# Kernel tuning notes

Measured on AMD Instinct MI355X. Metric: run time of the kernel, lower is better.

The kernel has to match this reference:

```python
import jax, jax.numpy as jnp
import numpy as np

DIM = 768
HEADS = 12
HEAD_DIM = DIM // HEADS
SCALE = HEAD_DIM ** (-0.5)
BATCH = 1
SEQ = 4096


def setup_inputs() -> dict:
    key = jax.random.key(0)
    ks = jax.random.split(key, 5)
    x = jax.random.normal(ks[0], (BATCH, SEQ, DIM), dtype=jnp.float32)
    # Linear params stored (in, out) for y = x @ W + b
    w_qkv = jax.random.normal(ks[1], (DIM, 3 * DIM), dtype=jnp.float32) * (DIM ** -0.5)
    b_qkv = jnp.zeros((3 * DIM,), dtype=jnp.float32)
    w_proj = jax.random.normal(ks[2], (DIM, DIM), dtype=jnp.float32) * (DIM ** -0.5)
    b_proj = jnp.zeros((DIM,), dtype=jnp.float32)
    return {"x": x, "w_qkv": w_qkv, "b_qkv": b_qkv, "w_proj": w_proj, "b_proj": b_proj}


def reference(x, w_qkv, b_qkv, w_proj, b_proj):
    B, S, _ = x.shape
    qkv = x @ w_qkv + b_qkv                              # [B,S,3*DIM]
    qkv = qkv.reshape(B, S, 3, HEADS, HEAD_DIM)
    q, k, v = qkv[:, :, 0], qkv[:, :, 1], qkv[:, :, 2]   # [B,S,H,D]
    # scaled dot-product attention, full score matrix as in the original
    attn = jnp.einsum("bqhd,bkhd->bhqk", q * SCALE, k)   # [B,H,S,S]
    attn = jax.nn.softmax(attn, axis=-1)
    out = jnp.einsum("bhqk,bkhd->bqhd", attn, v)         # [B,S,H,D]
    out = out.reshape(B, S, DIM)
    return out @ w_proj + b_proj
```

## Files before the change

kernel.cpp:

```cpp
#include <hip/hip_runtime.h>
#include <hip/hip_bf16.h>

#define SEQ   4096
#define DIM   768
#define HEADS 12
#define NQKV  2304
#define QSCALE 0.18033688011f

#if __has_builtin(__builtin_amdgcn_exp2f)
#define EXP2(x) __builtin_amdgcn_exp2f(x)
#else
#define EXP2(x) __expf((x) * 0.69314718056f)
#endif

typedef __bf16 bf16_t;
typedef bf16_t bf16x8 __attribute__((ext_vector_type(8)));
typedef float  f32x4  __attribute__((ext_vector_type(4)));
typedef float  f32x16 __attribute__((ext_vector_type(16)));
typedef unsigned short u16;
typedef unsigned int   u32;

static __device__ __forceinline__ float bf2f(u16 v) {
    union { float f; unsigned u; } x; x.u = ((unsigned)v) << 16; return x.f;
}
static __device__ __forceinline__ u16 f2bf(float f) {
    union { float f; unsigned u; } x; x.f = f;
    unsigned r = x.u + 0x7fff + ((x.u >> 16) & 1);
    return (u16)(r >> 16);
}
static __device__ __forceinline__ u32 fbits(float f) {
    union { float f; unsigned u; } x; x.f = f; return x.u;
}
static __device__ __forceinline__ void gload_lds16(const u16* g, u16* l) {
    __builtin_amdgcn_global_load_lds(
        (const __attribute__((address_space(1))) unsigned int*)g,
        (__attribute__((address_space(3))) unsigned int*)l, 16, 0, 0);
}

static __device__ __forceinline__ int detect_f32(const u32* __restrict__ x) {
    int lane = threadIdx.x & 63;
    int cnt = 0;
#pragma unroll
    for (int i = 0; i < 8; ++i) {
        u32 w = x[lane * 8 + i];
        cnt += (((w >> 7) & 0xFF) >= 0x8F) ? 1 : 0;
    }
#pragma unroll
    for (int m = 1; m < 64; m <<= 1) cnt += __shfl_xor(cnt, m);
    return cnt >= 64;
}

__global__ __launch_bounds__(256) void prep(
    const void* __restrict__ x, const void* __restrict__ wqkv,
    const void* __restrict__ bqkv, const void* __restrict__ wproj,
    const void* __restrict__ bproj,
    u16* __restrict__ cvt, u16* __restrict__ wqkvT, u16* __restrict__ wprojT)
{
    __shared__ u16 tile[64][65];
    const bool f32 = detect_f32((const u32*)x) != 0;
    const int b = blockIdx.x;
    const int t = threadIdx.x;

    if (b < 576) {
        const void* src; u16* dst; int K, N, tx, ty;
        if (b < 432) { src = wqkv; dst = wqkvT; K = DIM; N = NQKV; tx = b % 36; ty = b / 36; }
        else { int bb = b - 432; src = wproj; dst = wprojT; K = DIM; N = DIM; tx = bb % 12; ty = bb / 12; }
        const int k0 = ty * 64, n0 = tx * 64;
#pragma unroll
        for (int i = 0; i < 4; ++i) {
            int idx = i * 256 + t;
            int r = idx >> 4, c4 = (idx & 15) * 4;
            size_t si = (size_t)(k0 + r) * N + n0 + c4;
            if (f32) {
                float4 v = *(const float4*)((const float*)src + si);
                tile[r][c4 + 0] = f2bf(v.x); tile[r][c4 + 1] = f2bf(v.y);
                tile[r][c4 + 2] = f2bf(v.z); tile[r][c4 + 3] = f2bf(v.w);
            } else {
                ushort4 v = *(const ushort4*)((const u16*)src + si);
                tile[r][c4 + 0] = v.x; tile[r][c4 + 1] = v.y;
                tile[r][c4 + 2] = v.z; tile[r][c4 + 3] = v.w;
            }
        }
        __syncthreads();
#pragma unroll
        for (int i = 0; i < 2; ++i) {
            int idx = i * 256 + t;
            int r = idx >> 3, c0 = (idx & 7) * 8;
            union { u16 u[8]; bf16x8 v; } pk;
#pragma unroll
            for (int j = 0; j < 8; ++j) pk.u[j] = tile[c0 + j][r];
            *(bf16x8*)(dst + (size_t)(n0 + r) * K + k0 + c0) = pk.v;
        }
    } else {
        const int SX = SEQ * DIM;
        const int gid = (b - 576) * 256 + t;
        for (int i = gid; i < SX / 8; i += 200 * 256) {
            if (f32) {
                float4 v0 = *((const float4*)x + (size_t)i * 2);
                float4 v1 = *((const float4*)x + (size_t)i * 2 + 1);
                union { u16 u[8]; bf16x8 v; } pk;
                pk.u[0] = f2bf(v0.x); pk.u[1] = f2bf(v0.y);
                pk.u[2] = f2bf(v0.z); pk.u[3] = f2bf(v0.w);
                pk.u[4] = f2bf(v1.x); pk.u[5] = f2bf(v1.y);
                pk.u[6] = f2bf(v1.z); pk.u[7] = f2bf(v1.w);
                *((bf16x8*)cvt + i) = pk.v;
            } else {
                *((bf16x8*)cvt + i) = *((const bf16x8*)x + i);
            }
        }
        if (gid < NQKV + DIM) {
            const void* s; int off;
            if (gid < NQKV) { s = bqkv;  off = gid; }
            else            { s = bproj; off = gid - NQKV; }
            cvt[SX + gid] = f32 ? f2bf(((const float*)s)[off]) : ((const u16*)s)[off];
        }
    }
}

template<int MODE, int BM, int BN>
__global__ __launch_bounds__(256) void gemm128(
    const u16* __restrict__ A, const u16* __restrict__ BT, const u16* __restrict__ bias,
    u16* __restrict__ C0, float* __restrict__ Cf, u16* __restrict__ VT,
    const u32* __restrict__ xdet, int M, int N, int K)
{
    constexpr int WM  = BM / 2;
    constexpr int WN  = BN / 2;
    constexpr int NI  = WM / 16;
    constexpr int NJ  = WN / 16;
    constexpr int ARW = BM / 4;
    constexpr int BRW = BN / 4;
    constexpr int LPS = (BM + BN) / 64;
    constexpr int TSTR = BM + 8;

    __shared__ union SharedLds {
        struct { u16 a[3][BM * 32]; u16 b[3][BN * 32]; } s;
        u16 t[(MODE == 1) ? 128 * TSTR : 1];
    } lds;

    const int t    = threadIdx.x;
    const int w    = t >> 6;
    const int lane = t & 63;
    const int l15  = lane & 15;
    const int quad = lane >> 4;
    const int wm   = w >> 1, wn = w & 1;

    const int lin     = blockIdx.y * gridDim.x + blockIdx.x;
    const int cpx     = (gridDim.x * gridDim.y) >> 3;
    const int logical = (lin & 7) * cpx + (lin >> 3);
    const int m0 = (logical / gridDim.x) * BM;
    const int n0 = (logical % gridDim.x) * BN;

    const int kch = (lane & 3) * 8;
    const u16* asrc = A  + (size_t)(m0 + w * ARW + (lane >> 2)) * K + kch;
    const u16* bsrc = BT + (size_t)(n0 + w * BRW + (lane >> 2)) * K + kch;
    const int woffA = w * ARW * 32;
    const int woffB = w * BRW * 32;

    f32x4 acc[NI][NJ] = {};

    u16 *aA = lds.s.a[0], *aB = lds.s.a[1], *aC = lds.s.a[2];
    u16 *bA = lds.s.b[0], *bB = lds.s.b[1], *bC = lds.s.b[2];

    auto STAGE = [&](u16* ad, u16* bd) {
#pragma unroll
        for (int s = 0; s < BM / 64; ++s)
            gload_lds16(asrc + s * 16 * K, ad + woffA + s * 16 * 32);
#pragma unroll
        for (int s = 0; s < BN / 64; ++s)
            gload_lds16(bsrc + s * 16 * K, bd + woffB + s * 16 * 32);
        asrc += 32; bsrc += 32;
    };
    auto COMPUTE = [&](const u16* ab_, const u16* bb_) {
        const u16* ab = ab_ + (wm * WM + l15) * 32 + quad * 8;
        const u16* bb = bb_ + (wn * WN + l15) * 32 + quad * 8;
        bf16x8 af[NI], bfr[NJ];
#pragma unroll
        for (int i = 0; i < NI; ++i) af[i]  = *(const bf16x8*)(ab + i * 16 * 32);
#pragma unroll
        for (int j = 0; j < NJ; ++j) bfr[j] = *(const bf16x8*)(bb + j * 16 * 32);
#pragma unroll
        for (int i = 0; i < NI; ++i)
#pragma unroll
            for (int j = 0; j < NJ; ++j)
                acc[i][j] = __builtin_amdgcn_mfma_f32_16x16x32_bf16(af[i], bfr[j], acc[i][j], 0, 0, 0);
    };
    auto WAIT_LPS = [&]() {
        if constexpr (LPS == 4)      asm volatile("s_waitcnt vmcnt(4)" ::: "memory");
        else if constexpr (LPS == 3) asm volatile("s_waitcnt vmcnt(3)" ::: "memory");
        else                         asm volatile("s_waitcnt vmcnt(2)" ::: "memory");
    };

    const int NK = K >> 5;
    STAGE(aA, bA);
    STAGE(aB, bB);
    for (int kt = 0; kt < NK - 2; ++kt) {
        WAIT_LPS();
        __builtin_amdgcn_s_barrier();
        STAGE(aC, bC);
        COMPUTE(aA, bA);
        { u16* tt = aA; aA = aB; aB = aC; aC = tt; }
        { u16* tt = bA; bA = bB; bB = bC; bC = tt; }
    }
    WAIT_LPS();
    __builtin_amdgcn_s_barrier();
    COMPUTE(aA, bA);
    { u16* tt = aA; aA = aB; aB = aC; aC = tt; }
    { u16* tt = bA; bA = bB; bB = bC; bC = tt; }
    asm volatile("s_waitcnt vmcnt(0)" ::: "memory");
    __builtin_amdgcn_s_barrier();
    COMPUTE(aA, bA);

    if constexpr (MODE == 1) {
        if (n0 >= 1536) {
            __syncthreads();
#pragma unroll
            for (int i = 0; i < NI; ++i)
#pragma unroll
                for (int j = 0; j < NJ; ++j)
#pragma unroll
                    for (int r = 0; r < 4; ++r) {
                        int ml = wm * WM + i * 16 + quad * 4 + r;
                        int nl = wn * WN + j * 16 + l15;
                        int mpl = (ml & ~15) | (ml & 3) |
                                  (((ml >> 2) & 1) << 3) | (((ml >> 3) & 1) << 2);
                        float v = acc[i][j][r] + bf2f(bias[n0 + nl]);
                        lds.t[nl * TSTR + mpl] = f2bf(v);
                    }
            __syncthreads();
            constexpr int LPR = BM / 8;
            constexpr int RPP = 256 / LPR;
            const int rr = t / LPR;
            const int mo = (t % LPR) * 8;
#pragma unroll
            for (int it = 0; it < 128 / RPP; ++it) {
                int nl = rr + it * RPP;
                *(bf16x8*)(VT + (size_t)(n0 - 1536 + nl) * SEQ + m0 + mo) =
                    *(const bf16x8*)(lds.t + nl * TSTR + mo);
            }
            return;
        }
    }

    bool outf32 = false;
    if (MODE == 0) outf32 = detect_f32(xdet) != 0;
#pragma unroll
    for (int i = 0; i < NI; ++i)
#pragma unroll
        for (int j = 0; j < NJ; ++j)
#pragma unroll
            for (int r = 0; r < 4; ++r) {
                int m = m0 + wm * WM + i * 16 + quad * 4 + r;
                int n = n0 + wn * WN + j * 16 + l15;
                float v = acc[i][j][r] + bf2f(bias[n]);
                if (MODE == 0) {
                    if (outf32) Cf[(size_t)m * N + n] = v;
                    else        C0[(size_t)m * N + n] = f2bf(v);
                } else {
                    float s = (n < 768) ? v * QSCALE : v;
                    C0[(size_t)m * 1536 + n] = f2bf(s);
                }
            }
}

__global__ __launch_bounds__(256, 3) void attn_kernel(
    const u16* __restrict__ qk, const u16* __restrict__ vt, u16* __restrict__ out)
{
    __shared__ u16 k_lds[3][64 * 64];
    __shared__ u16 v_lds[3][64 * 64];
    __shared__ float l_red[2][2][32];

    const int t    = threadIdx.x;
    const int w    = t >> 6;
    const int lane = t & 63;
    const int l31  = lane & 31;
    const int h    = lane >> 5;
    const int wq   = w & 1;
    const int wk   = w >> 1;

    const int lin     = blockIdx.x + (blockIdx.y << 6);
    const int logical = (lin & 7) * 96 + (lin >> 3);
    const int head    = logical >> 6;
    const int q0      = (logical & 63) * 64 + wq * 32;

    const u16* qrow = qk + (size_t)(q0 + l31) * 1536 + head * 64 + h * 8;
    bf16x8 qb[4];
#pragma unroll
    for (int s = 0; s < 4; ++s) qb[s] = *(const bf16x8*)(qrow + 16 * s);

    bf16x8 ones;
#pragma unroll
    for (int j = 0; j < 8; ++j) ones[j] = (bf16_t)1.0f;

    const f32x16 fz = {};

    const int srow = 8 * w + (lane >> 3);
    const int cs   = ((lane & 7) - srow) & 7;
    const u16* kst0 = qk + 768 + head * 64 + (size_t)srow * 1536 + cs * 8;
    const u16* kst1 = kst0 + (size_t)32 * 1536;
    const u16* vst0 = vt + (size_t)head * 64 * SEQ + (size_t)srow * SEQ + cs * 8;
    const u16* vst1 = vst0 + (size_t)32 * SEQ;
    const int woff = 8 * w * 64;

    const int krow = 32 * wk + l31;

    f32x16 o0 = {}, o1 = {}, lac = {};

    auto SK = [&](u16* kd) {
        gload_lds16(kst0, kd + woff);
        gload_lds16(kst1, kd + woff + 32 * 64);
        kst0 += (size_t)64 * 1536;
        kst1 += (size_t)64 * 1536;
    };
    auto SV = [&](u16* vd) {
        gload_lds16(vst0, vd + woff);
        gload_lds16(vst1, vd + woff + 32 * 64);
        vst0 += 64;
        vst1 += 64;
    };

    auto QK = [&](const u16* kb) -> f32x16 {
        const u16* kbase = kb + krow * 64;
        bf16x8 ka0 = *(const bf16x8*)(kbase + (((0 + h + krow) & 7) * 8));
        bf16x8 ka1 = *(const bf16x8*)(kbase + (((2 + h + krow) & 7) * 8));
        bf16x8 ka2 = *(const bf16x8*)(kbase + (((4 + h + krow) & 7) * 8));
        bf16x8 ka3 = *(const bf16x8*)(kbase + (((6 + h + krow) & 7) * 8));
        __builtin_amdgcn_s_setprio(1);
        f32x16 st = __builtin_amdgcn_mfma_f32_32x32x16_bf16(ka0, qb[0], fz, 0, 0, 0);
        st = __builtin_amdgcn_mfma_f32_32x32x16_bf16(ka1, qb[1], st, 0, 0, 0);
        st = __builtin_amdgcn_mfma_f32_32x32x16_bf16(ka2, qb[2], st, 0, 0, 0);
        st = __builtin_amdgcn_mfma_f32_32x32x16_bf16(ka3, qb[3], st, 0, 0, 0);
        __builtin_amdgcn_s_setprio(0);
        return st;
    };

    auto SMPV = [&](const f32x16& st, const u16* vb) {
        u32 q32[8];
#pragma unroll
        for (int i = 0; i < 8; ++i) {
            float pe = EXP2(st[2 * i]);
            float po = EXP2(st[2 * i + 1]);
            q32[i] = __builtin_amdgcn_perm(fbits(po), fbits(pe), 0x07060302u);
        }
        union { u32 u[4]; bf16x8 v; } pf0, pf1;
#pragma unroll
        for (int i = 0; i < 4; ++i) { pf0.u[i] = q32[i]; pf1.u[i] = q32[4 + i]; }
        __builtin_amdgcn_s_setprio(1);
#pragma unroll
        for (int s2 = 0; s2 < 2; ++s2) {
            const int c = 4 * wk + 2 * s2 + h;
            bf16x8 vb0 = *(const bf16x8*)(vb + l31 * 64 + (((c + l31) & 7) * 8));
            bf16x8 vb1 = *(const bf16x8*)(vb + (32 + l31) * 64 + (((c + 32 + l31) & 7) * 8));
            const bf16x8 pv = s2 ? pf1.v : pf0.v;
            o0  = __builtin_amdgcn_mfma_f32_32x32x16_bf16(pv, vb0, o0, 0, 0, 0);
            o1  = __builtin_amdgcn_mfma_f32_32x32x16_bf16(pv, vb1, o1, 0, 0, 0);
            lac = __builtin_amdgcn_mfma_f32_32x32x16_bf16(pv, ones, lac, 0, 0, 0);
        }
        __builtin_amdgcn_s_setprio(0);
    };

    u16 *kA = &k_lds[0][0], *kB = &k_lds[1][0], *kC = &k_lds[2][0];
    u16 *vA = &v_lds[0][0], *vB = &v_lds[1][0], *vC = &v_lds[2][0];

    SK(kA);
    SV(vA);
    SK(kB);
    asm volatile("s_waitcnt vmcnt(4)" ::: "memory");
    __builtin_amdgcn_s_barrier();
    f32x16 stA = QK(kA);
    SV(vB);
    f32x16 stB;

    for (int i = 0; i < 31; ++i) {
        SK(kC);
        asm volatile("s_waitcnt vmcnt(4)" ::: "memory");
        __builtin_amdgcn_s_barrier();
        stB = QK(kB);
        SMPV(stA, vA);
        SV(vC);
        { u16* tt = kA; kA = kB; kB = kC; kC = tt; }
        { u16* tt = vA; vA = vB; vB = vC; vC = tt; }
        SK(kC);
        asm volatile("s_waitcnt vmcnt(4)" ::: "memory");
        __builtin_amdgcn_s_barrier();
        stA = QK(kB);
        SMPV(stB, vA);
        SV(vC);
        { u16* tt = kA; kA = kB; kB = kC; kC = tt; }
        { u16* tt = vA; vA = vB; vB = vC; vC = tt; }
    }
    asm volatile("s_waitcnt vmcnt(2)" ::: "memory");
    __builtin_amdgcn_s_barrier();
    stB = QK(kB);
    SMPV(stA, vA);
    { u16* tt = kA; kA = kB; kB = kC; kC = tt; }
    { u16* tt = vA; vA = vB; vB = vC; vC = tt; }
    asm volatile("s_waitcnt vmcnt(0)" ::: "memory");
    __builtin_amdgcn_s_barrier();
    SMPV(stB, vA);
    __syncthreads();

    if (l31 == 0) {
#pragma unroll
        for (int r = 0; r < 16; ++r) {
            int row = (r & 3) + 8 * (r >> 2) + 4 * h;
            l_red[wq][wk][row] = lac[r];
        }
    }
    float* scr = (wq == 0) ? (float*)&k_lds[0][0] : (float*)&v_lds[0][0];
    if (wk == 1) {
#pragma unroll
        for (int r = 0; r < 16; ++r) {
            int row = (r & 3) + 8 * (r >> 2) + 4 * h;
            scr[row * 64 + l31]      = o0[r];
            scr[row * 64 + 32 + l31] = o1[r];
        }
    }
    __syncthreads();
    if (wk == 0) {
#pragma unroll
        for (int r = 0; r < 16; ++r) {
            int row = (r & 3) + 8 * (r >> 2) + 4 * h;
            float lt   = l_red[wq][0][row] + l_red[wq][1][row];
            float invl = 1.0f / lt;
            float s0 = o0[r] + scr[row * 64 + l31];
            float s1 = o1[r] + scr[row * 64 + 32 + l31];
            size_t gr = (size_t)(q0 + row) * 768 + head * 64;
            out[gr + l31]      = f2bf(s0 * invl);
            out[gr + 32 + l31] = f2bf(s1 * invl);
        }
    }
}

extern "C" void kernel_launch(void* const* d_in, const int* in_sizes, int n_in,
                              void* d_out, int out_size, void* d_ws, size_t ws_size,
                              hipStream_t stream) {
    const int SX = SEQ * DIM;

    u16* base   = (u16*)d_ws;
    u16* xb     = base;
    u16* bqkvb  = xb + SX;
    u16* bprojb = bqkvb + NQKV;
    u16* wqkvT  = bprojb + DIM;
    u16* wprojT = wqkvT + (size_t)NQKV * DIM;
    u16* qkb    = wprojT + (size_t)DIM * DIM;
    u16* vtb    = qkb + (size_t)SEQ * 1536;
    u16* attnb  = xb;

    prep<<<776, 256, 0, stream>>>(
        d_in[0], d_in[1], d_in[2], d_in[3], d_in[4], base, wqkvT, wprojT);
    gemm128<1, 128, 128><<<dim3(NQKV / 128, SEQ / 128), 256, 0, stream>>>(
        xb, wqkvT, bqkvb, qkb, nullptr, vtb, (const u32*)d_in[0],
        SEQ, NQKV, DIM);
    attn_kernel<<<dim3(SEQ / 64, HEADS), 256, 0, stream>>>(qkb, vtb, attnb);
    gemm128<0, 128, 128><<<dim3(DIM / 128, SEQ / 128), 256, 0, stream>>>(
        attnb, wprojT, bprojb, (u16*)d_out, (float*)d_out, nullptr,
        (const u32*)d_in[0], SEQ, DIM, DIM);
}
```

Baseline: 190.4 us.

## Make QKV GEMM persistent with atomic tile counter scheduling

The QKV projection GEMM now launches 512 persistent workgroups that pull 128x128 output tiles from a global atomic counter, instead of one workgroup per tile (576 tiles). The counter is reset inside the prep kernel. This targets the tail-wave imbalance of the 576-tile grid. In exchange it adds an atomic and two barriers per tile, and tiles are now visited in plain row-major order, dropping the previous XCD-aware swizzle, which may hurt L2 locality.

```diff
diff --git a/kernel.cpp b/kernel.cpp
--- a/kernel.cpp
+++ b/kernel.cpp
@@ -54,12 +54,15 @@
     const void* __restrict__ x, const void* __restrict__ wqkv,
     const void* __restrict__ bqkv, const void* __restrict__ wproj,
     const void* __restrict__ bproj,
-    u16* __restrict__ cvt, u16* __restrict__ wqkvT, u16* __restrict__ wprojT)
+    u16* __restrict__ cvt, u16* __restrict__ wqkvT, u16* __restrict__ wprojT,
+    u32* __restrict__ ctr)
 {
     __shared__ u16 tile[64][65];
     const bool f32 = detect_f32((const u32*)x) != 0;
     const int b = blockIdx.x;
     const int t = threadIdx.x;
+
+    if (b == 0 && t == 0) *ctr = 0;
 
     if (b < 576) {
         const void* src; u16* dst; int K, N, tx, ty;
@@ -117,11 +120,11 @@
     }
 }
 
-template<int MODE, int BM, int BN>
+template<int MODE, int BM, int BN, int PERSIST>
 __global__ __launch_bounds__(256) void gemm128(
     const u16* __restrict__ A, const u16* __restrict__ BT, const u16* __restrict__ bias,
     u16* __restrict__ C0, float* __restrict__ Cf, u16* __restrict__ VT,
-    const u32* __restrict__ xdet, int M, int N, int K)
+    const u32* __restrict__ xdet, u32* __restrict__ ctr, int M, int N, int K)
 {
     constexpr int WM  = BM / 2;
     constexpr int WN  = BN / 2;
@@ -136,6 +139,7 @@
         struct { u16 a[3][BM * 32]; u16 b[3][BN * 32]; } s;
         u16 t[(MODE == 1) ? 128 * TSTR : 1];
     } lds;
+    __shared__ u32 s_tile;
 
     const int t    = threadIdx.x;
     const int w    = t >> 6;
@@ -143,75 +147,94 @@
     const int l15  = lane & 15;
     const int quad = lane >> 4;
     const int wm   = w >> 1, wn = w & 1;
-
-    const int lin     = blockIdx.y * gridDim.x + blockIdx.x;
-    const int cpx     = (gridDim.x * gridDim.y) >> 3;
-    const int logical = (lin & 7) * cpx + (lin >> 3);
-    const int m0 = (logical / gridDim.x) * BM;
-    const int n0 = (logical % gridDim.x) * BN;
-
-    const int kch = (lane & 3) * 8;
-    const u16* asrc = A  + (size_t)(m0 + w * ARW + (lane >> 2)) * K + kch;
-    const u16* bsrc = BT + (size_t)(n0 + w * BRW + (lane >> 2)) * K + kch;
+    const int kch  = (lane & 3) * 8;
     const int woffA = w * ARW * 32;
     const int woffB = w * BRW * 32;
 
-    f32x4 acc[NI][NJ] = {};
-
-    u16 *aA = lds.s.a[0], *aB = lds.s.a[1], *aC = lds.s.a[2];
-    u16 *bA = lds.s.b[0], *bB = lds.s.b[1], *bC = lds.s.b[2];
-
-    auto STAGE = [&](u16* ad, u16* bd) {
-#pragma unroll
-        for (int s = 0; s < BM / 64; ++s)
-            gload_lds16(asrc + s * 16 * K, ad + woffA + s * 16 * 32);
-#pragma unroll
-        for (int s = 0; s < BN / 64; ++s)
-            gload_lds16(bsrc + s * 16 * K, bd + woffB + s * 16 * 32);
-        asrc += 32; bsrc += 32;
-    };
-    auto COMPUTE = [&](const u16* ab_, const u16* bb_) {
-        const u16* ab = ab_ + (wm * WM + l15) * 32 + quad * 8;
-        const u16* bb = bb_ + (wn * WN + l15) * 32 + quad * 8;
-        bf16x8 af[NI], bfr[NJ];
-#pragma unroll
-        for (int i = 0; i < NI; ++i) af[i]  = *(const bf16x8*)(ab + i * 16 * 32);
-#pragma unroll
-        for (int j = 0; j < NJ; ++j) bfr[j] = *(const bf16x8*)(bb + j * 16 * 32);
-#pragma unroll
-        for (int i = 0; i < NI; ++i)
-#pragma unroll
-            for (int j = 0; j < NJ; ++j)
-                acc[i][j] = __builtin_amdgcn_mfma_f32_16x16x32_bf16(af[i], bfr[j], acc[i][j], 0, 0, 0);
-    };
-    auto WAIT_LPS = [&]() {
-        if constexpr (LPS == 4)      asm volatile("s_waitcnt vmcnt(4)" ::: "memory");
-        else if constexpr (LPS == 3) asm volatile("s_waitcnt vmcnt(3)" ::: "memory");
-        else                         asm volatile("s_waitcnt vmcnt(2)" ::: "memory");
-    };
-
-    const int NK = K >> 5;
-    STAGE(aA, bA);
-    STAGE(aB, bB);
-    for (int kt = 0; kt < NK - 2; ++kt) {
+    const int ntn = N / BN;
+    const int NT  = (M / BM) * ntn;
+
+    bool outf32 = false;
+    if (MODE == 0) outf32 = detect_f32(xdet) != 0;
+
+    for (;;) {
+        int m0, n0;
+        if constexpr (PERSIST) {
+            if (t == 0) s_tile = atomicAdd(ctr, 1u);
+            __syncthreads();
+            const u32 tile = s_tile;
+            __syncthreads();
+            if (tile >= (u32)NT) return;
+            m0 = (int)(tile / (u32)ntn) * BM;
+            n0 = (int)(tile % (u32)ntn) * BN;
+        } else {
+            const int lin = blockIdx.y * gridDim.x + blockIdx.x;
+            const int cpx = (gridDim.x * gridDim.y) >> 3;
+            const int logical = (lin & 7) * cpx + (lin >> 3);
+            m0 = (logical / gridDim.x) * BM;
+            n0 = (logical % gridDim.x) * BN;
+        }
+
+        const u16* asrc = A  + (size_t)(m0 + w * ARW + (lane >> 2)) * K + kch;
+        const u16* bsrc = BT + (size_t)(n0 + w * BRW + (lane >> 2)) * K + kch;
+
+        f32x4 acc[NI][NJ] = {};
+
+        u16 *aA = lds.s.a[0], *aB = lds.s.a[1], *aC = lds.s.a[2];
+        u16 *bA = lds.s.b[0], *bB = lds.s.b[1], *bC = lds.s.b[2];
+
+        auto STAGE = [&](u16* ad, u16* bd) {
+#pragma unroll
+            for (int s = 0; s < BM / 64; ++s)
+                gload_lds16(asrc + s * 16 * K, ad + woffA + s * 16 * 32);
+#pragma unroll
+            for (int s = 0; s < BN / 64; ++s)
+                gload_lds16(bsrc + s * 16 * K, bd + woffB + s * 16 * 32);
+            asrc += 32; bsrc += 32;
+        };
+        auto COMPUTE = [&](const u16* ab_, const u16* bb_) {
+            const u16* ab = ab_ + (wm * WM + l15) * 32 + quad * 8;
+            const u16* bb = bb_ + (wn * WN + l15) * 32 + quad * 8;
+            bf16x8 af[NI], bfr[NJ];
+#pragma unroll
+            for (int i = 0; i < NI; ++i) af[i]  = *(const bf16x8*)(ab + i * 16 * 32);
+#pragma unroll
+            for (int j = 0; j < NJ; ++j) bfr[j] = *(const bf16x8*)(bb + j * 16 * 32);
+#pragma unroll
+            for (int i = 0; i < NI; ++i)
+#pragma unroll
+                for (int j = 0; j < NJ; ++j)
+                    acc[i][j] = __builtin_amdgcn_mfma_f32_16x16x32_bf16(af[i], bfr[j], acc[i][j], 0, 0, 0);
+        };
+        auto WAIT_LPS = [&]() {
+            if constexpr (LPS == 4)      asm volatile("s_waitcnt vmcnt(4)" ::: "memory");
+            else if constexpr (LPS == 3) asm volatile("s_waitcnt vmcnt(3)" ::: "memory");
+            else                         asm volatile("s_waitcnt vmcnt(2)" ::: "memory");
+        };
+
+        const int NK = K >> 5;
+        STAGE(aA, bA);
+        STAGE(aB, bB);
+        for (int kt = 0; kt < NK - 2; ++kt) {
+            WAIT_LPS();
+            __builtin_amdgcn_s_barrier();
+            STAGE(aC, bC);
+            COMPUTE(aA, bA);
+            { u16* tt = aA; aA = aB; aB = aC; aC = tt; }
+            { u16* tt = bA; bA = bB; bB = bC; bC = tt; }
+        }
         WAIT_LPS();
         __builtin_amdgcn_s_barrier();
-        STAGE(aC, bC);
         COMPUTE(aA, bA);
         { u16* tt = aA; aA = aB; aB = aC; aC = tt; }
         { u16* tt = bA; bA = bB; bB = bC; bC = tt; }
-    }
-    WAIT_LPS();
-    __builtin_amdgcn_s_barrier();
-    COMPUTE(aA, bA);
-    { u16* tt = aA; aA = aB; aB = aC; aC = tt; }
-    { u16* tt = bA; bA = bB; bB = bC; bC = tt; }
-    asm volatile("s_waitcnt vmcnt(0)" ::: "memory");
-    __builtin_amdgcn_s_barrier();
-    COMPUTE(aA, bA);
-
-    if constexpr (MODE == 1) {
-        if (n0 >= 1536) {
+        asm volatile("s_waitcnt vmcnt(0)" ::: "memory");
+        __builtin_amdgcn_s_barrier();
+        COMPUTE(aA, bA);
+
+        bool vpath = false;
+        if constexpr (MODE == 1) vpath = (n0 >= 1536);
+        if (vpath) {
             __syncthreads();
 #pragma unroll
             for (int i = 0; i < NI; ++i)
@@ -237,29 +260,28 @@
                 *(bf16x8*)(VT + (size_t)(n0 - 1536 + nl) * SEQ + m0 + mo) =
                     *(const bf16x8*)(lds.t + nl * TSTR + mo);
             }
-            return;
-        }
-    }
-
-    bool outf32 = false;
-    if (MODE == 0) outf32 = detect_f32(xdet) != 0;
-#pragma unroll
-    for (int i = 0; i < NI; ++i)
-#pragma unroll
-        for (int j = 0; j < NJ; ++j)
-#pragma unroll
-            for (int r = 0; r < 4; ++r) {
-                int m = m0 + wm * WM + i * 16 + quad * 4 + r;
-                int n = n0 + wn * WN + j * 16 + l15;
-                float v = acc[i][j][r] + bf2f(bias[n]);
-                if (MODE == 0) {
-                    if (outf32) Cf[(size_t)m * N + n] = v;
-                    else        C0[(size_t)m * N + n] = f2bf(v);
-                } else {
-                    float s = (n < 768) ? v * QSCALE : v;
-                    C0[(size_t)m * 1536 + n] = f2bf(s);
-                }
-            }
+        } else {
+#pragma unroll
+            for (int i = 0; i < NI; ++i)
+#pragma unroll
+                for (int j = 0; j < NJ; ++j)
+#pragma unroll
+                    for (int r = 0; r < 4; ++r) {
+                        int m = m0 + wm * WM + i * 16 + quad * 4 + r;
+                        int n = n0 + wn * WN + j * 16 + l15;
+                        float v = acc[i][j][r] + bf2f(bias[n]);
+                        if (MODE == 0) {
+                            if (outf32) Cf[(size_t)m * N + n] = v;
+                            else        C0[(size_t)m * N + n] = f2bf(v);
+                        } else {
+                            float s = (n < 768) ? v * QSCALE : v;
+                            C0[(size_t)m * 1536 + n] = f2bf(s);
+                        }
+                    }
+        }
+
+        if constexpr (!PERSIST) return;
+    }
 }
 
 __global__ __launch_bounds__(256, 3) void attn_kernel(
@@ -444,15 +466,16 @@
     u16* wprojT = wqkvT + (size_t)NQKV * DIM;
     u16* qkb    = wprojT + (size_t)DIM * DIM;
     u16* vtb    = qkb + (size_t)SEQ * 1536;
+    u32* ctr    = (u32*)(vtb + (size_t)HEADS * 64 * SEQ);
     u16* attnb  = xb;
 
     prep<<<776, 256, 0, stream>>>(
-        d_in[0], d_in[1], d_in[2], d_in[3], d_in[4], base, wqkvT, wprojT);
-    gemm128<1, 128, 128><<<dim3(NQKV / 128, SEQ / 128), 256, 0, stream>>>(
-        xb, wqkvT, bqkvb, qkb, nullptr, vtb, (const u32*)d_in[0],
+        d_in[0], d_in[1], d_in[2], d_in[3], d_in[4], base, wqkvT, wprojT, ctr);
+    gemm128<1, 128, 128, 1><<<512, 256, 0, stream>>>(
+        xb, wqkvT, bqkvb, qkb, nullptr, vtb, (const u32*)d_in[0], ctr,
         SEQ, NQKV, DIM);
     attn_kernel<<<dim3(SEQ / 64, HEADS), 256, 0, stream>>>(qkb, vtb, attnb);
-    gemm128<0, 128, 128><<<dim3(DIM / 128, SEQ / 128), 256, 0, stream>>>(
+    gemm128<0, 128, 128, 0><<<dim3(DIM / 128, SEQ / 128), 256, 0, stream>>>(
         attnb, wprojT, bprojb, (u16*)d_out, (float*)d_out, nullptr,
-        (const u32*)d_in[0], SEQ, DIM, DIM);
-}
+        (const u32*)d_in[0], ctr, SEQ, DIM, DIM);
+}
```

New measurement: 207.3 us. 8.9% more time.
